# Kernel tuning notes

Hardware: AMD Instinct MI355X
Metric: run time of the kernel (lower is better)

Reference implementation:

```python
import jax, jax.numpy as jnp
import numpy as np

D_MODEL = 1024
EXPAND = 2
D_INNER = D_MODEL * EXPAND  # 2048
D_STATE = 16
D_CONV = 4
DT_RANK = (D_MODEL + 15) // 16  # 64
BATCH = 2
SEQ = 1024


def setup_inputs() -> dict:
    key = jax.random.key(0)
    ks = jax.random.split(key, 10)
    s = lambda d: 1.0 / np.sqrt(d)
    x = jax.random.normal(ks[0], (BATCH, SEQ, D_MODEL), dtype=jnp.float32)
    W_in = jax.random.normal(ks[1], (D_MODEL, 2 * D_INNER), dtype=jnp.float32) * s(D_MODEL)
    conv_w = jax.random.normal(ks[2], (D_INNER, D_CONV), dtype=jnp.float32) * s(D_CONV)
    conv_b = jax.random.normal(ks[3], (D_INNER,), dtype=jnp.float32) * 0.02
    W_x = jax.random.normal(ks[4], (D_INNER, DT_RANK + 2 * D_STATE), dtype=jnp.float32) * s(D_INNER)
    W_dt = jax.random.normal(ks[5], (DT_RANK, D_INNER), dtype=jnp.float32) * s(DT_RANK)
    b_dt = jax.random.uniform(ks[6], (D_INNER,), dtype=jnp.float32, minval=-4.0, maxval=-2.0)
    # S4D-real init: A = -[1..d_state] per channel
    A_log = jnp.log(jnp.tile(jnp.arange(1, D_STATE + 1, dtype=jnp.float32), (D_INNER, 1)))
    D = jnp.ones((D_INNER,), dtype=jnp.float32)
    W_out = jax.random.normal(ks[7], (D_INNER, D_MODEL), dtype=jnp.float32) * s(D_INNER)
    return {"x": x, "W_in": W_in, "conv_w": conv_w, "conv_b": conv_b,
            "W_x": W_x, "W_dt": W_dt, "b_dt": b_dt, "A_log": A_log,
            "D": D, "W_out": W_out}


def _mamba_forward(x, W_in, conv_w, conv_b, W_x, W_dt, b_dt, A_log, D, W_out):
    B, L, _ = x.shape
    # input projection -> [B, L, 2*d_inner], split into u (conv branch) and z (gate)
    xz = jnp.einsum('bld,de->ble', x, W_in)
    u, z = jnp.split(xz, 2, axis=-1)  # each [B, L, d_inner]

    # causal depthwise conv over time
    u_c = jnp.transpose(u, (0, 2, 1))                      # [B, d_inner, L]
    u_c = jnp.pad(u_c, ((0, 0), (0, 0), (D_CONV - 1, 0)))  # left pad for causality
    kern = conv_w[:, None, :]                              # [d_inner, 1, d_conv]
    u_c = jax.lax.conv_general_dilated(
        u_c, kern, window_strides=(1,), padding='VALID',
        dimension_numbers=('NCH', 'OIH', 'NCH'),
        feature_group_count=D_INNER)
    u_c = u_c + conv_b[None, :, None]
    u_c = jax.nn.silu(jnp.transpose(u_c, (0, 2, 1)))       # [B, L, d_inner]

    # data-dependent SSM parameters
    x_dbl = jnp.einsum('bld,de->ble', u_c, W_x)            # [B, L, dt_rank+2*d_state]
    dt_lowrank = x_dbl[..., :DT_RANK]
    Bmat = x_dbl[..., DT_RANK:DT_RANK + D_STATE]           # [B, L, d_state]
    Cmat = x_dbl[..., DT_RANK + D_STATE:]                  # [B, L, d_state]
    dt = jax.nn.softplus(jnp.einsum('blr,rd->bld', dt_lowrank, W_dt) + b_dt)

    A = -jnp.exp(A_log)                                    # [d_inner, d_state]

    # selective scan over time: h' = exp(dt*A) h + dt*B*u ; y = <h, C>
    def step(h, inp):
        u_t, dt_t, B_t, C_t = inp                          # [B,d], [B,d], [B,n], [B,n]
        dA = jnp.exp(dt_t[..., None] * A)                  # [B, d_inner, d_state]
        dBu = (dt_t * u_t)[..., None] * B_t[:, None, :]    # [B, d_inner, d_state]
        h = dA * h + dBu
        y_t = jnp.einsum('bdn,bn->bd', h, C_t)
        return h, y_t

    h0 = jnp.zeros((B, D_INNER, D_STATE), dtype=x.dtype)
    seq = (jnp.swapaxes(u_c, 0, 1), jnp.swapaxes(dt, 0, 1),
           jnp.swapaxes(Bmat, 0, 1), jnp.swapaxes(Cmat, 0, 1))
    _, ys = jax.lax.scan(step, h0, seq)                    # ys: [L, B, d_inner]
    y = jnp.swapaxes(ys, 0, 1) + u_c * D                   # skip term
    y = y * jax.nn.silu(z)                                 # gate
    return jnp.einsum('bld,de->ble', y, W_out)             # [B, L, d_model]


def reference(x, W_in, conv_w, conv_b, W_x, W_dt, b_dt, A_log, D, W_out):
    return _mamba_forward(x, W_in, conv_w, conv_b, W_x, W_dt, b_dt, A_log, D, W_out)
```

## Files before the change

kernel.cpp:

```cpp
#include <hip/hip_runtime.h>
#include <hip/hip_bf16.h>


typedef __attribute__((ext_vector_type(8))) short bfrag;
typedef __attribute__((ext_vector_type(4))) float f32x4;

#define CF   32
#define CLEN 32

__device__ __forceinline__ unsigned short f2bf(float f) {
    unsigned int u = __float_as_uint(f);
    u += 0x7FFF + ((u >> 16) & 1);
    return (unsigned short)(u >> 16);
}
__device__ __forceinline__ float bf2f(unsigned short s) {
    return __uint_as_float((unsigned int)s << 16);
}

__device__ __forceinline__ void async_copy16(const unsigned short* g,
                                             unsigned short* l) {
    __builtin_amdgcn_global_load_lds(
        (const __attribute__((address_space(1))) void*)g,
        (__attribute__((address_space(3))) void*)l, 16, 0, 0);
}

template<int MT>
__global__ __launch_bounds__(256) void gemm_bf16_v2(
    const unsigned short* __restrict__ A,
    const unsigned short* __restrict__ BT,
    float* __restrict__ C,
    unsigned short* __restrict__ C1,
    int K, int lda, int ldb, int ldc, int split)
{
    constexpr int FI  = MT / 32;
    constexpr int ACH = MT / 32;
    __shared__ __align__(16) unsigned short sA[MT * 64];
    __shared__ __align__(16) unsigned short sB[128 * 64];

    const int tid  = threadIdx.x;
    const int wave = tid >> 6, lane = tid & 63;
    const int lm   = lane & 15;
    const int quad = lane >> 4;
    const int wrow = (wave >> 1) * (MT / 2);
    const int wcol = (wave & 1) * 64;
    const int bm = blockIdx.y * MT, bn = blockIdx.x * 128;

    const int lrow = lane >> 3;
    const int lkb  = (lane & 7) ^ lrow;

    f32x4 acc[FI][4];
    #pragma unroll
    for (int i = 0; i < FI; ++i)
        #pragma unroll
        for (int j = 0; j < 4; ++j) {
            acc[i][j][0] = 0.f; acc[i][j][1] = 0.f;
            acc[i][j][2] = 0.f; acc[i][j][3] = 0.f;
        }

    for (int k0 = 0; k0 < K; k0 += 64) {
        #pragma unroll
        for (int c = 0; c < ACH; ++c) {
            const int chunk = wave * ACH + c;
            const int row = chunk * 8 + lrow;
            async_copy16(&A[(size_t)(bm + row) * lda + k0 + lkb * 8],
                         &sA[chunk * 512 + lane * 8]);
        }
        #pragma unroll
        for (int c = 0; c < 4; ++c) {
            const int chunk = wave * 4 + c;
            const int row = chunk * 8 + lrow;
            async_copy16(&BT[(size_t)(bn + row) * ldb + k0 + lkb * 8],
                         &sB[chunk * 512 + lane * 8]);
        }
        __syncthreads();

        #pragma unroll
        for (int ks = 0; ks < 2; ++ks) {
            bfrag af[FI], bf[4];
            #pragma unroll
            for (int i = 0; i < FI; ++i) {
                const int row = wrow + i * 16 + lm;
                const int slot = (ks * 4 + quad) ^ (row & 7);
                af[i] = *(const bfrag*)&sA[row * 64 + slot * 8];
            }
            #pragma unroll
            for (int j = 0; j < 4; ++j) {
                const int row = wcol + j * 16 + lm;
                const int slot = (ks * 4 + quad) ^ (row & 7);
                bf[j] = *(const bfrag*)&sB[row * 64 + slot * 8];
            }
            #pragma unroll
            for (int i = 0; i < FI; ++i)
                #pragma unroll
                for (int j = 0; j < 4; ++j)
                    acc[i][j] = __builtin_amdgcn_mfma_f32_16x16x32_bf16(
                        af[i], bf[j], acc[i][j], 0, 0, 0);
        }
        __syncthreads();
    }

    #pragma unroll
    for (int i = 0; i < FI; ++i)
        #pragma unroll
        for (int j = 0; j < 4; ++j) {
            const int col = bn + wcol + j * 16 + lm;
            #pragma unroll
            for (int r = 0; r < 4; ++r) {
                const int row = bm + wrow + i * 16 + quad * 4 + r;
                float v = acc[i][j][r];
                if (split > 0) {
                    if (col < split) C [(size_t)row * split + col] = v;
                    else             C1[(size_t)row * split + (col - split)] = f2bf(v);
                } else {
                    C[(size_t)row * ldc + col] = v;
                }
            }
        }
}

__global__ __launch_bounds__(256) void transpose_cast(
    const float* __restrict__ in, unsigned short* __restrict__ out,
    int rows, int cols)
{
    __shared__ float tile[32][33];
    const int j0 = blockIdx.x * 32, i0 = blockIdx.y * 32;
    const int tx = threadIdx.x & 31, ty = threadIdx.x >> 5;
    #pragma unroll
    for (int k = 0; k < 4; ++k)
        tile[ty + 8 * k][tx] = in[(size_t)(i0 + ty + 8 * k) * cols + j0 + tx];
    __syncthreads();
    #pragma unroll
    for (int k = 0; k < 4; ++k)
        out[(size_t)(j0 + ty + 8 * k) * rows + i0 + tx] = f2bf(tile[tx][ty + 8 * k]);
}

__global__ __launch_bounds__(256) void cast_bf16(
    const float* __restrict__ in, unsigned short* __restrict__ out)
{
    int i = (blockIdx.x * 256 + threadIdx.x) * 4;
    float4 v = *(const float4*)&in[i];
    ushort4 o;
    o.x = f2bf(v.x); o.y = f2bf(v.y); o.z = f2bf(v.z); o.w = f2bf(v.w);
    *(ushort4*)&out[i] = o;
}

#define SK_KS 128
__global__ __launch_bounds__(256) void gemm_f32_splitk(
    const float* __restrict__ A, const float* __restrict__ B,
    float* __restrict__ part)
{
    __shared__ __align__(16) float As[16][64];
    __shared__ __align__(16) float Bs[16][96];

    const int tid = threadIdx.x;
    const int mtile = blockIdx.x >> 4;
    const int kslice = blockIdx.x & 15;
    const int bm = mtile * 64;
    const int kbase = kslice * SK_KS;

    const int am = tid >> 2;
    const int ak = (tid & 3) << 2;

    const int ty = tid >> 4, tx = tid & 15;
    const int rm = ty << 2;
    const int rn = tx * 6;

    float acc[4][6] = {};

    for (int k0 = 0; k0 < SK_KS; k0 += 16) {
        float4 av = *(const float4*)&A[(size_t)(bm + am) * 2048 + kbase + k0 + ak];
        As[ak + 0][am] = av.x;
        As[ak + 1][am] = av.y;
        As[ak + 2][am] = av.z;
        As[ak + 3][am] = av.w;
        for (int i = tid; i < 384; i += 256) {
            int br = i / 24, bc = (i % 24) << 2;
            *(float4*)&Bs[br][bc] = *(const float4*)&B[(size_t)(kbase + k0 + br) * 96 + bc];
        }
        __syncthreads();

        #pragma unroll
        for (int k = 0; k < 16; ++k) {
            float4 a = *(const float4*)&As[k][rm];
            float b[6];
            #pragma unroll
            for (int j = 0; j < 6; ++j) b[j] = Bs[k][rn + j];
            #pragma unroll
            for (int j = 0; j < 6; ++j) {
                acc[0][j] += a.x * b[j];
                acc[1][j] += a.y * b[j];
                acc[2][j] += a.z * b[j];
                acc[3][j] += a.w * b[j];
            }
        }
        __syncthreads();
    }

    float* pout = part + (size_t)kslice * 196608;
    #pragma unroll
    for (int i = 0; i < 4; ++i) {
        float* crow = pout + (size_t)(bm + rm + i) * 96 + rn;
        #pragma unroll
        for (int j = 0; j < 6; ++j)
            crow[j] = acc[i][j];
    }
}

__global__ __launch_bounds__(256) void reduce_splitk(
    const float* __restrict__ part, float* __restrict__ xdbl)
{
    int i = (blockIdx.x * 256 + threadIdx.x) * 4;
    float4 acc = {0.f, 0.f, 0.f, 0.f};
    #pragma unroll
    for (int s = 0; s < 16; ++s) {
        float4 v = *(const float4*)&part[(size_t)s * 196608 + i];
        acc.x += v.x; acc.y += v.y; acc.z += v.z; acc.w += v.w;
    }
    *(float4*)&xdbl[i] = acc;
}

#define BM 64
#define BN 64
#define BK 16
__global__ __launch_bounds__(256) void gemm_f32(
    const float* __restrict__ A, const float* __restrict__ B,
    float* __restrict__ C, int M, int N, int K,
    int lda, int ldb, int ldc, int mode, const float* __restrict__ bias)
{
    __shared__ __align__(16) float As[BK][BM];
    __shared__ __align__(16) float Bs[BK][BN];

    const int tid = threadIdx.x;
    const int bm = blockIdx.y * BM;
    const int bn = blockIdx.x * BN;

    const int am = tid >> 2;
    const int ak = (tid & 3) << 2;
    const int bk = tid >> 4;
    const int bnn = (tid & 15) << 2;

    const int tx = tid & 15, ty = tid >> 4;
    const int rm = ty << 2;
    const int rn = tx << 2;
    const int cm = bm + rm, cn = bn + rn;

    float acc[4][4] = {};

    for (int k0 = 0; k0 < K; k0 += BK) {
        const float* ap = A + (size_t)(bm + am) * lda + (k0 + ak);
        float4 av = *(const float4*)ap;
        As[ak + 0][am] = av.x;
        As[ak + 1][am] = av.y;
        As[ak + 2][am] = av.z;
        As[ak + 3][am] = av.w;
        {
            const int ncol = bn + bnn;
            const float* bp = B + (size_t)(k0 + bk) * ldb + ncol;
            float4 bv;
            if (ncol + 3 < N) {
                bv = *(const float4*)bp;
            } else {
                bv.x = (ncol + 0 < N) ? bp[0] : 0.f;
                bv.y = (ncol + 1 < N) ? bp[1] : 0.f;
                bv.z = (ncol + 2 < N) ? bp[2] : 0.f;
                bv.w = (ncol + 3 < N) ? bp[3] : 0.f;
            }
            *(float4*)&Bs[bk][bnn] = bv;
        }
        __syncthreads();

        #pragma unroll
        for (int k = 0; k < BK; ++k) {
            float4 a = *(const float4*)&As[k][rm];
            float4 b = *(const float4*)&Bs[k][rn];
            acc[0][0] += a.x * b.x; acc[0][1] += a.x * b.y;
            acc[0][2] += a.x * b.z; acc[0][3] += a.x * b.w;
            acc[1][0] += a.y * b.x; acc[1][1] += a.y * b.y;
            acc[1][2] += a.y * b.z; acc[1][3] += a.y * b.w;
            acc[2][0] += a.z * b.x; acc[2][1] += a.z * b.y;
            acc[2][2] += a.z * b.z; acc[2][3] += a.z * b.w;
            acc[3][0] += a.w * b.x; acc[3][1] += a.w * b.y;
            acc[3][2] += a.w * b.z; acc[3][3] += a.w * b.w;
        }
        __syncthreads();
    }

    #pragma unroll
    for (int i = 0; i < 4; ++i) {
        float* crow = C + (size_t)(cm + i) * ldc;
        #pragma unroll
        for (int j = 0; j < 4; ++j) {
            int col = cn + j;
            if (col < N) {
                float v = acc[i][j];
                if (mode == 1) {
                    v += bias[col];
                    v = (v > 20.f) ? v : logf(1.f + expf(v));
                }
                crow[col] = v;
            }
        }
    }
}

__global__ __launch_bounds__(256) void conv_silu_kernel(
    const float* __restrict__ upre, const float* __restrict__ cw,
    const float* __restrict__ cb, float* __restrict__ uc)
{
    int idx = blockIdx.x * 256 + threadIdx.x;
    int d = idx & 2047;
    int r = idx >> 11;
    int l = r & 1023;

    float4 w4 = *(const float4*)(cw + 4 * d);
    float w[4] = { w4.x, w4.y, w4.z, w4.w };
    float acc = cb[d];
    const float* up = upre + (size_t)r * 2048 + d;
    if (l >= 3) {
        acc += w[0] * up[-3 * 2048] + w[1] * up[-2 * 2048]
             + w[2] * up[-1 * 2048] + w[3] * up[0];
    } else {
        #pragma unroll
        for (int j = 0; j < 4; ++j) {
            int lj = l - 3 + j;
            if (lj >= 0) acc += w[j] * up[(j - 3) * 2048];
        }
    }
    float sig = 1.f / (1.f + expf(-acc));
    uc[idx] = acc * sig;
}

__global__ __launch_bounds__(256) void scan_pass1(
    const float* __restrict__ uc,
    const float* __restrict__ dtb,
    const float* __restrict__ xdbl,
    const float* __restrict__ A_log,
    float* __restrict__ Hend,
    float* __restrict__ Sdt)
{
    __shared__ float sB[CLEN][16];
    const int tid = threadIdx.x;
    const int bx  = blockIdx.x;
    const int c   = bx & (CF - 1);
    const int g   = (bx >> 5) & 7;
    const int b   = bx >> 8;
    const int d   = g * 256 + tid;
    const size_t rowbase = (size_t)b * 1024 + c * CLEN;

    for (int i = tid; i < CLEN * 16; i += 256) {
        int tt = i >> 4, nn = i & 15;
        sB[tt][nn] = xdbl[(rowbase + tt) * 96 + 64 + nn];
    }

    float A2[16];
    {
        float al[16];
        #pragma unroll
        for (int q = 0; q < 4; ++q)
            *(float4*)&al[4 * q] = *(const float4*)&A_log[(size_t)d * 16 + 4 * q];
        #pragma unroll
        for (int n = 0; n < 16; ++n) A2[n] = -expf(al[n]) * 1.44269504f;
    }
    __syncthreads();

    float h[16];
    #pragma unroll
    for (int n = 0; n < 16; ++n) h[n] = 0.f;
    float sdt = 0.f;

    #pragma unroll 4
    for (int t = 0; t < CLEN; ++t) {
        size_t r = rowbase + t;
        float dtv = dtb[r * 2048 + d];
        float uv  = uc [r * 2048 + d];
        sdt += dtv;
        float dtu = dtv * uv;
        float bl[16];
        #pragma unroll
        for (int q = 0; q < 4; ++q)
            *(float4*)&bl[4 * q] = *(const float4*)&sB[t][4 * q];
        #pragma unroll
        for (int n = 0; n < 16; ++n)
            h[n] = exp2f(dtv * A2[n]) * h[n] + dtu * bl[n];
    }

    size_t base = ((size_t)(b * CF + c) * 2048 + d) * 16;
    #pragma unroll
    for (int q = 0; q < 4; ++q)
        *(float4*)&Hend[base + 4 * q] = *(float4*)&h[4 * q];
    Sdt[(size_t)(b * CF + c) * 2048 + d] = sdt;
}

__global__ __launch_bounds__(256) void scan_pass2(
    const float* __restrict__ Hend, const float* __restrict__ Sdt,
    const float* __restrict__ A_log, float* __restrict__ Hin)
{
    int gid = blockIdx.x * 256 + threadIdx.x;
    int b = gid >> 15;
    int rest = gid & 32767;
    int d = rest >> 4;
    float A2 = -expf(A_log[rest]) * 1.44269504f;
    float H = 0.f;
    #pragma unroll
    for (int c = 0; c < CF; ++c) {
        size_t sidx = (size_t)(b * CF + c) * 2048 + d;
        size_t idx  = ((size_t)(b * CF + c) << 15) + rest;
        Hin[idx] = H;
        H = exp2f(A2 * Sdt[sidx]) * H + Hend[idx];
    }
}

__global__ __launch_bounds__(256) void scan_pass3(
    const float* __restrict__ uc,
    const float* __restrict__ dtb,
    const unsigned short* __restrict__ zb,
    const float* __restrict__ xdbl,
    const float* __restrict__ A_log,
    const float* __restrict__ Dvec,
    const float* __restrict__ Hin,
    unsigned short* __restrict__ yb)
{
    __shared__ float sBC[CLEN][32];
    const int tid = threadIdx.x;
    const int bx  = blockIdx.x;
    const int c   = bx & (CF - 1);
    const int g   = (bx >> 5) & 7;
    const int b   = bx >> 8;
    const int d   = g * 256 + tid;
    const size_t rowbase = (size_t)b * 1024 + c * CLEN;

    for (int i = tid; i < CLEN * 32; i += 256) {
        int tt = i >> 5, j = i & 31;
        sBC[tt][j] = xdbl[(rowbase + tt) * 96 + 64 + j];
    }

    float A2[16];
    {
        float al[16];
        #pragma unroll
        for (int q = 0; q < 4; ++q)
            *(float4*)&al[4 * q] = *(const float4*)&A_log[(size_t)d * 16 + 4 * q];
        #pragma unroll
        for (int n = 0; n < 16; ++n) A2[n] = -expf(al[n]) * 1.44269504f;
    }
    const float Dd = Dvec[d];

    float h[16];
    {
        size_t base = ((size_t)(b * CF + c) * 2048 + d) * 16;
        #pragma unroll
        for (int q = 0; q < 4; ++q)
            *(float4*)&h[4 * q] = *(const float4*)&Hin[base + 4 * q];
    }
    __syncthreads();

    #pragma unroll 2
    for (int t = 0; t < CLEN; ++t) {
        size_t r = rowbase + t;
        float dtv = dtb[r * 2048 + d];
        float uv  = uc [r * 2048 + d];
        float zv  = bf2f(zb[r * 2048 + d]);
        float dtu = dtv * uv;
        float bl[16], cl[16];
        #pragma unroll
        for (int q = 0; q < 4; ++q) {
            *(float4*)&bl[4 * q] = *(const float4*)&sBC[t][4 * q];
            *(float4*)&cl[4 * q] = *(const float4*)&sBC[t][16 + 4 * q];
        }
        float acc = uv * Dd;
        #pragma unroll
        for (int n = 0; n < 16; ++n) {
            h[n] = exp2f(dtv * A2[n]) * h[n] + dtu * bl[n];
            acc += h[n] * cl[n];
        }
        float yv = acc * zv / (1.f + expf(-zv));
        yb[r * 2048 + d] = f2bf(yv);
    }
}

extern "C" void kernel_launch(void* const* d_in, const int* in_sizes, int n_in,
                              void* d_out, int out_size, void* d_ws, size_t ws_size,
                              hipStream_t stream)
{
    const float* x      = (const float*)d_in[0];
    const float* W_in   = (const float*)d_in[1];
    const float* conv_w = (const float*)d_in[2];
    const float* conv_b = (const float*)d_in[3];
    const float* W_x    = (const float*)d_in[4];
    const float* W_dt   = (const float*)d_in[5];
    const float* b_dt   = (const float*)d_in[6];
    const float* A_log  = (const float*)d_in[7];
    const float* Dv     = (const float*)d_in[8];
    const float* W_out  = (const float*)d_in[9];
    float* out = (float*)d_out;

    float* ws    = (float*)d_ws;
    float* upre  = ws;
    float* dtb   = upre;
    float* uc    = ws + 4194304;
    float* xdbl  = uc + 4194304;
    float* Hend  = xdbl + 196608;
    float* Hin   = Hend + 2097152;
    float* Sdt   = Hin + 2097152;
    float* part  = Hend;
    unsigned short* zb   = (unsigned short*)(Sdt + 131072);
    unsigned short* xb   = zb + 4194304;
    unsigned short* wbT  = xb + 2097152;
    unsigned short* wobT = wbT + 4194304;
    unsigned short* yb   = wbT;

    dim3 blk(256);

    transpose_cast<<<dim3(128, 32), blk, 0, stream>>>(W_in, wbT, 1024, 4096);
    transpose_cast<<<dim3(32, 64), blk, 0, stream>>>(W_out, wobT, 2048, 1024);
    cast_bf16<<<2048, blk, 0, stream>>>(x, xb);

    gemm_bf16_v2<128><<<dim3(32, 16), blk, 0, stream>>>(
        xb, wbT, upre, zb, 1024, 1024, 1024, 0, 2048);

    conv_silu_kernel<<<(2048 * 2048) / 256, blk, 0, stream>>>(upre, conv_w, conv_b, uc);

    gemm_f32_splitk<<<512, blk, 0, stream>>>(uc, W_x, part);
    reduce_splitk<<<192, blk, 0, stream>>>(part, xdbl);

    gemm_f32<<<dim3(32, 32), blk, 0, stream>>>(
        xdbl, W_dt, dtb, 2048, 2048, 64, 96, 2048, 2048, 1, b_dt);

    scan_pass1<<<512, blk, 0, stream>>>(uc, dtb, xdbl, A_log, Hend, Sdt);
    scan_pass2<<<256, blk, 0, stream>>>(Hend, Sdt, A_log, Hin);
    scan_pass3<<<512, blk, 0, stream>>>(uc, dtb, zb, xdbl, A_log, Dv, Hin, yb);

    gemm_bf16_v2<64><<<dim3(8, 32), blk, 0, stream>>>(
        yb, wobT, out, nullptr, 2048, 2048, 2048, 1024, 0);
}
```

Baseline: 281.2 us.

## Store conv output and dt in bf16, retile output GEMM to 64x64

```diff
diff --git a/kernel.cpp b/kernel.cpp
--- a/kernel.cpp
+++ b/kernel.cpp
@@ -24,7 +24,7 @@
         (__attribute__((address_space(3))) void*)l, 16, 0, 0);
 }
 
-template<int MT>
+template<int MT, int NT>
 __global__ __launch_bounds__(256) void gemm_bf16_v2(
     const unsigned short* __restrict__ A,
     const unsigned short* __restrict__ BT,
@@ -33,26 +33,28 @@
     int K, int lda, int ldb, int ldc, int split)
 {
     constexpr int FI  = MT / 32;
+    constexpr int FJ  = NT / 32;
     constexpr int ACH = MT / 32;
+    constexpr int BCH = NT / 32;
     __shared__ __align__(16) unsigned short sA[MT * 64];
-    __shared__ __align__(16) unsigned short sB[128 * 64];
+    __shared__ __align__(16) unsigned short sB[NT * 64];
 
     const int tid  = threadIdx.x;
     const int wave = tid >> 6, lane = tid & 63;
     const int lm   = lane & 15;
     const int quad = lane >> 4;
     const int wrow = (wave >> 1) * (MT / 2);
-    const int wcol = (wave & 1) * 64;
-    const int bm = blockIdx.y * MT, bn = blockIdx.x * 128;
+    const int wcol = (wave & 1) * (NT / 2);
+    const int bm = blockIdx.y * MT, bn = blockIdx.x * NT;
 
     const int lrow = lane >> 3;
     const int lkb  = (lane & 7) ^ lrow;
 
-    f32x4 acc[FI][4];
+    f32x4 acc[FI][FJ];
     #pragma unroll
     for (int i = 0; i < FI; ++i)
         #pragma unroll
-        for (int j = 0; j < 4; ++j) {
+        for (int j = 0; j < FJ; ++j) {
             acc[i][j][0] = 0.f; acc[i][j][1] = 0.f;
             acc[i][j][2] = 0.f; acc[i][j][3] = 0.f;
         }
@@ -66,8 +68,8 @@
                          &sA[chunk * 512 + lane * 8]);
         }
         #pragma unroll
-        for (int c = 0; c < 4; ++c) {
-            const int chunk = wave * 4 + c;
+        for (int c = 0; c < BCH; ++c) {
+            const int chunk = wave * BCH + c;
             const int row = chunk * 8 + lrow;
             async_copy16(&BT[(size_t)(bn + row) * ldb + k0 + lkb * 8],
                          &sB[chunk * 512 + lane * 8]);
@@ -76,7 +78,7 @@
 
         #pragma unroll
         for (int ks = 0; ks < 2; ++ks) {
-            bfrag af[FI], bf[4];
+            bfrag af[FI], bf[FJ];
             #pragma unroll
             for (int i = 0; i < FI; ++i) {
                 const int row = wrow + i * 16 + lm;
@@ -84,7 +86,7 @@
                 af[i] = *(const bfrag*)&sA[row * 64 + slot * 8];
             }
             #pragma unroll
-            for (int j = 0; j < 4; ++j) {
+            for (int j = 0; j < FJ; ++j) {
                 const int row = wcol + j * 16 + lm;
                 const int slot = (ks * 4 + quad) ^ (row & 7);
                 bf[j] = *(const bfrag*)&sB[row * 64 + slot * 8];
@@ -92,7 +94,7 @@
             #pragma unroll
             for (int i = 0; i < FI; ++i)
                 #pragma unroll
-                for (int j = 0; j < 4; ++j)
+                for (int j = 0; j < FJ; ++j)
                     acc[i][j] = __builtin_amdgcn_mfma_f32_16x16x32_bf16(
                         af[i], bf[j], acc[i][j], 0, 0, 0);
         }
@@ -102,7 +104,7 @@
     #pragma unroll
     for (int i = 0; i < FI; ++i)
         #pragma unroll
-        for (int j = 0; j < 4; ++j) {
+        for (int j = 0; j < FJ; ++j) {
             const int col = bn + wcol + j * 16 + lm;
             #pragma unroll
             for (int r = 0; r < 4; ++r) {
@@ -146,7 +148,8 @@
 
 #define SK_KS 128
 __global__ __launch_bounds__(256) void gemm_f32_splitk(
-    const float* __restrict__ A, const float* __restrict__ B,
+    const unsigned short* __restrict__ A,
+    const float* __restrict__ B,
     float* __restrict__ part)
 {
     __shared__ __align__(16) float As[16][64];
@@ -168,11 +171,11 @@
     float acc[4][6] = {};
 
     for (int k0 = 0; k0 < SK_KS; k0 += 16) {
-        float4 av = *(const float4*)&A[(size_t)(bm + am) * 2048 + kbase + k0 + ak];
-        As[ak + 0][am] = av.x;
-        As[ak + 1][am] = av.y;
-        As[ak + 2][am] = av.z;
-        As[ak + 3][am] = av.w;
+        ushort4 av = *(const ushort4*)&A[(size_t)(bm + am) * 2048 + kbase + k0 + ak];
+        As[ak + 0][am] = bf2f(av.x);
+        As[ak + 1][am] = bf2f(av.y);
+        As[ak + 2][am] = bf2f(av.z);
+        As[ak + 3][am] = bf2f(av.w);
         for (int i = tid; i < 384; i += 256) {
             int br = i / 24, bc = (i % 24) << 2;
             *(float4*)&Bs[br][bc] = *(const float4*)&B[(size_t)(kbase + k0 + br) * 96 + bc];
@@ -287,7 +290,6 @@
 
     #pragma unroll
     for (int i = 0; i < 4; ++i) {
-        float* crow = C + (size_t)(cm + i) * ldc;
         #pragma unroll
         for (int j = 0; j < 4; ++j) {
             int col = cn + j;
@@ -296,8 +298,10 @@
                 if (mode == 1) {
                     v += bias[col];
                     v = (v > 20.f) ? v : logf(1.f + expf(v));
+                    ((unsigned short*)C)[(size_t)(cm + i) * ldc + col] = f2bf(v);
+                } else {
+                    C[(size_t)(cm + i) * ldc + col] = v;
                 }
-                crow[col] = v;
             }
         }
     }
@@ -305,7 +309,7 @@
 
 __global__ __launch_bounds__(256) void conv_silu_kernel(
     const float* __restrict__ upre, const float* __restrict__ cw,
-    const float* __restrict__ cb, float* __restrict__ uc)
+    const float* __restrict__ cb, unsigned short* __restrict__ uc)
 {
     int idx = blockIdx.x * 256 + threadIdx.x;
     int d = idx & 2047;
@@ -327,12 +331,12 @@
         }
     }
     float sig = 1.f / (1.f + expf(-acc));
-    uc[idx] = acc * sig;
+    uc[idx] = f2bf(acc * sig);
 }
 
 __global__ __launch_bounds__(256) void scan_pass1(
-    const float* __restrict__ uc,
-    const float* __restrict__ dtb,
+    const unsigned short* __restrict__ uc,
+    const unsigned short* __restrict__ dtb,
     const float* __restrict__ xdbl,
     const float* __restrict__ A_log,
     float* __restrict__ Hend,
@@ -371,8 +375,8 @@
     #pragma unroll 4
     for (int t = 0; t < CLEN; ++t) {
         size_t r = rowbase + t;
-        float dtv = dtb[r * 2048 + d];
-        float uv  = uc [r * 2048 + d];
+        float dtv = bf2f(dtb[r * 2048 + d]);
+        float uv  = bf2f(uc [r * 2048 + d]);
         sdt += dtv;
         float dtu = dtv * uv;
         float bl[16];
@@ -411,8 +415,8 @@
 }
 
 __global__ __launch_bounds__(256) void scan_pass3(
-    const float* __restrict__ uc,
-    const float* __restrict__ dtb,
+    const unsigned short* __restrict__ uc,
+    const unsigned short* __restrict__ dtb,
     const unsigned short* __restrict__ zb,
     const float* __restrict__ xdbl,
     const float* __restrict__ A_log,
@@ -457,9 +461,9 @@
     #pragma unroll 2
     for (int t = 0; t < CLEN; ++t) {
         size_t r = rowbase + t;
-        float dtv = dtb[r * 2048 + d];
-        float uv  = uc [r * 2048 + d];
-        float zv  = bf2f(zb[r * 2048 + d]);
+        float dtv = bf2f(dtb[r * 2048 + d]);
+        float uv  = bf2f(uc [r * 2048 + d]);
+        float zv  = bf2f(zb [r * 2048 + d]);
         float dtu = dtv * uv;
         float bl[16], cl[16];
         #pragma unroll
@@ -496,9 +500,9 @@
 
     float* ws    = (float*)d_ws;
     float* upre  = ws;
-    float* dtb   = upre;
-    float* uc    = ws + 4194304;
-    float* xdbl  = uc + 4194304;
+    unsigned short* dtb = (unsigned short*)upre;
+    unsigned short* uc = (unsigned short*)(ws + 4194304);
+    float* xdbl  = ws + 4194304 + 2097152;
     float* Hend  = xdbl + 196608;
     float* Hin   = Hend + 2097152;
     float* Sdt   = Hin + 2097152;
@@ -515,7 +519,7 @@
     transpose_cast<<<dim3(32, 64), blk, 0, stream>>>(W_out, wobT, 2048, 1024);
     cast_bf16<<<2048, blk, 0, stream>>>(x, xb);
 
-    gemm_bf16_v2<128><<<dim3(32, 16), blk, 0, stream>>>(
+    gemm_bf16_v2<128, 128><<<dim3(32, 16), blk, 0, stream>>>(
         xb, wbT, upre, zb, 1024, 1024, 1024, 0, 2048);
 
     conv_silu_kernel<<<(2048 * 2048) / 256, blk, 0, stream>>>(upre, conv_w, conv_b, uc);
@@ -524,12 +528,12 @@
     reduce_splitk<<<192, blk, 0, stream>>>(part, xdbl);
 
     gemm_f32<<<dim3(32, 32), blk, 0, stream>>>(
-        xdbl, W_dt, dtb, 2048, 2048, 64, 96, 2048, 2048, 1, b_dt);
+        xdbl, W_dt, (float*)dtb, 2048, 2048, 64, 96, 2048, 2048, 1, b_dt);
 
     scan_pass1<<<512, blk, 0, stream>>>(uc, dtb, xdbl, A_log, Hend, Sdt);
     scan_pass2<<<256, blk, 0, stream>>>(Hend, Sdt, A_log, Hin);
     scan_pass3<<<512, blk, 0, stream>>>(uc, dtb, zb, xdbl, A_log, Dv, Hin, yb);
 
-    gemm_bf16_v2<64><<<dim3(8, 32), blk, 0, stream>>>(
+    gemm_bf16_v2<64, 64><<<dim3(16, 32), blk, 0, stream>>>(
         yb, wobT, out, nullptr, 2048, 2048, 2048, 1024, 0);
 }
```

After: 271.8 us. 3.4% less time.
